# Optimization experiments

Hardware: AMD Instinct MI355X
Metric: run time of the kernel (lower is better)

## Reference

```python
import jax, jax.numpy as jnp
import numpy as np

B, S, E, H, D = 4, 2048, 1024, 16, 64


def setup_inputs() -> dict:
    key = jax.random.key(0)
    ks = jax.random.split(key, 6)
    scale_in = 1.0 / np.sqrt(E)
    return {
        "x": jax.random.normal(ks[0], (B, S, E), dtype=jnp.float32),
        "Wq": jax.random.normal(ks[1], (H, E, D), dtype=jnp.float32) * scale_in,
        "bq": jnp.zeros((H, D), dtype=jnp.float32),
        "Wk": jax.random.normal(ks[2], (H, E, D), dtype=jnp.float32) * scale_in,
        "bk": jnp.zeros((H, D), dtype=jnp.float32),
        "Wv": jax.random.normal(ks[3], (H, E, D), dtype=jnp.float32) * scale_in,
        "bv": jnp.zeros((H, D), dtype=jnp.float32),
        "Wo": jax.random.normal(ks[4], (H * D, E), dtype=jnp.float32) * (1.0 / np.sqrt(H * D)),
        "bo": jnp.zeros((E,), dtype=jnp.float32),
    }


def reference(x, Wq, bq, Wk, bk, Wv, bv, Wo, bo):
    # Per-head Q/K/V projections, batched over heads: [B,S,E] x [H,E,D] -> [B,H,S,D]
    q = jnp.einsum("bse,hed->bhsd", x, Wq) + bq[None, :, None, :]
    k = jnp.einsum("bse,hed->bhsd", x, Wk) + bk[None, :, None, :]
    v = jnp.einsum("bse,hed->bhsd", x, Wv) + bv[None, :, None, :]

    d = q.shape[-1]
    scores = jnp.einsum("bhqd,bhkd->bhqk", q, k) / jnp.sqrt(jnp.asarray(d, q.dtype))
    # Causal mask (registered tril buffer of size max_seq_len in HeadAttention)
    seq = scores.shape[-1]
    causal = jnp.tril(jnp.ones((seq, seq), dtype=bool))
    scores = jnp.where(causal[None, None, :, :], scores, jnp.asarray(-1e9, scores.dtype))
    attn = jax.nn.softmax(scores, axis=-1)
    out = jnp.einsum("bhqk,bhkd->bhqd", attn, v)  # [B,H,S,D]

    # Concat heads: [B,S,H*D], then output projection (dropout is identity in eval)
    out = out.transpose(0, 2, 1, 3).reshape(out.shape[0], out.shape[2], -1)
    return out @ Wo + bo
```

## Files before the change

kernel.cpp:

```cpp
#include <hip/hip_runtime.h>

typedef __bf16 bf16x8 __attribute__((ext_vector_type(8)));
typedef __bf16 bf16x4 __attribute__((ext_vector_type(4)));
typedef float  f32x4  __attribute__((ext_vector_type(4)));

#define B_    4
#define S_    2048
#define E_    1024
#define H_    16
#define D_    64
#define MROWS (B_*S_)
#define HD3   3072

#define SCORE_SCALE 0.18033688011112043f

__device__ __forceinline__ void load_lds16(const void* g, void* l) {
  __builtin_amdgcn_global_load_lds((__attribute__((address_space(1))) void*)g,
                                   (__attribute__((address_space(3))) void*)l,
                                   16, 0, 0);
}

__device__ __forceinline__ f32x4 mfma16(bf16x8 a, bf16x8 b, f32x4 c) {
  return __builtin_amdgcn_mfma_f32_16x16x32_bf16(a, b, c, 0, 0, 0);
}

__device__ __forceinline__ int swz(int row, int dchunk) {
  return row * 64 + ((dchunk ^ (row & 7)) * 8);
}


__global__ void prep(const float4* __restrict__ x, const float* __restrict__ Wq,
                     const float* __restrict__ Wk, const float* __restrict__ Wv,
                     const float* __restrict__ bq, const float* __restrict__ bk,
                     const float* __restrict__ bv, const float* __restrict__ Wo,
                     __bf16* __restrict__ xb, __bf16* __restrict__ Wt,
                     float* __restrict__ bqkv, __bf16* __restrict__ Wot) {
  __shared__ float t[64][65];
  int bid = blockIdx.x;
  if (bid < 8192) {
    int id = bid * 256 + threadIdx.x;
    float4 v = x[id];
    bf16x4 o = { (__bf16)v.x, (__bf16)v.y, (__bf16)v.z, (__bf16)v.w };
    *(bf16x4*)(xb + 4 * (size_t)id) = o;
    return;
  }
  int tx = threadIdx.x & 63;
  int ty = threadIdx.x >> 6;
  if (bid < 8960) {
    int b2 = bid - 8192;
    int e0 = (b2 & 15) * 64;
    int h  = (b2 >> 4) & 15;
    int p  = b2 >> 8;
    const float* W    = (p == 0) ? Wq : (p == 1) ? Wk : Wv;
    const float* bsrc = (p == 0) ? bq : (p == 1) ? bk : bv;
#pragma unroll
    for (int r = 0; r < 16; ++r) {
      int eL = ty + r * 4;
      t[eL][tx] = W[((size_t)h * 1024 + (e0 + eL)) * 64 + tx];
    }
    __syncthreads();
#pragma unroll
    for (int r = 0; r < 16; ++r) {
      int d = ty + r * 4;
      Wt[((size_t)(p * 1024 + h * 64 + d)) * 1024 + e0 + tx] = (__bf16)t[tx][d];
    }
    if ((b2 & 15) == 0 && threadIdx.x < 64)
      bqkv[p * 1024 + h * 64 + threadIdx.x] = bsrc[h * 64 + threadIdx.x];
  } else {
    int b2 = bid - 8960;
    int hd0 = (b2 >> 4) * 64;
    int e0  = (b2 & 15) * 64;
#pragma unroll
    for (int r = 0; r < 16; ++r) {
      int hdL = ty + r * 4;
      t[hdL][tx] = Wo[(size_t)(hd0 + hdL) * 1024 + e0 + tx];
    }
    __syncthreads();
#pragma unroll
    for (int r = 0; r < 16; ++r) {
      int eL = ty + r * 4;
      Wot[(size_t)(e0 + eL) * 1024 + hd0 + tx] = (__bf16)t[tx][eL];
    }
  }
}


template <int MODE>
__global__ __launch_bounds__(256) void gemm_bt(const __bf16* __restrict__ A,
                                               const __bf16* __restrict__ Bt,
                                               const float* __restrict__ bias,
                                               void* __restrict__ Cout,
                                               __bf16* __restrict__ VT,
                                               int M, int N, int K) {
  __shared__ __attribute__((aligned(16))) __bf16 As[128 * 64];
  __shared__ __attribute__((aligned(16))) __bf16 Bs[128 * 64];
  int tid = threadIdx.x, wave = tid >> 6, lane = tid & 63;
  int quad = lane >> 4, cc = lane & 15;
  int nb = N >> 7;
  int nwg = (int)gridDim.x;
  int bid = (int)blockIdx.x;
  bid = (bid & 7) * (nwg >> 3) + (bid >> 3);
  int bm = bid / nb, bn = bid % nb;
  const __bf16* Abase = A + (size_t)bm * 128 * K;
  const __bf16* Bbase = Bt + (size_t)bn * 128 * K;
  int wr = (wave >> 1) * 64, wc = (wave & 1) * 64;
  f32x4 acc[4][4];
#pragma unroll
  for (int i = 0; i < 4; ++i)
#pragma unroll
    for (int j = 0; j < 4; ++j) acc[i][j] = (f32x4){0.f, 0.f, 0.f, 0.f};

  int srow[4], scol[4];
#pragma unroll
  for (int p = 0; p < 4; ++p) {
    int g = tid + p * 256;
    srow[p] = g >> 3;
    scol[p] = ((g & 7) ^ (srow[p] & 7)) * 8;
  }
#pragma unroll
  for (int p = 0; p < 4; ++p) {
    load_lds16(Abase + (size_t)srow[p] * K + scol[p], &As[(tid + p * 256) * 8]);
    load_lds16(Bbase + (size_t)srow[p] * K + scol[p], &Bs[(tid + p * 256) * 8]);
  }

  for (int k0 = 0; k0 < K; k0 += 64) {
    __syncthreads();
    bf16x8 af[2][4], bf[2][4];
#pragma unroll
    for (int kk = 0; kk < 2; ++kk) {
#pragma unroll
      for (int i = 0; i < 4; ++i) af[kk][i] = *(const bf16x8*)&As[swz(wr + i * 16 + cc, kk * 4 + quad)];
#pragma unroll
      for (int j = 0; j < 4; ++j) bf[kk][j] = *(const bf16x8*)&Bs[swz(wc + j * 16 + cc, kk * 4 + quad)];
    }
    __syncthreads();
    if (k0 + 64 < K) {
      int kn = k0 + 64;
#pragma unroll
      for (int p = 0; p < 4; ++p) {
        load_lds16(Abase + (size_t)srow[p] * K + kn + scol[p], &As[(tid + p * 256) * 8]);
        load_lds16(Bbase + (size_t)srow[p] * K + kn + scol[p], &Bs[(tid + p * 256) * 8]);
      }
    }
#pragma unroll
    for (int kk = 0; kk < 2; ++kk)
#pragma unroll
      for (int i = 0; i < 4; ++i)
#pragma unroll
        for (int j = 0; j < 4; ++j) acc[i][j] = mfma16(af[kk][i], bf[kk][j], acc[i][j]);
  }

#pragma unroll
  for (int j = 0; j < 4; ++j) {
    int col = bn * 128 + wc + j * 16 + cc;
    float bv = bias[col];
#pragma unroll
    for (int i = 0; i < 4; ++i) {
      int row0 = bm * 128 + wr + i * 16 + quad * 4;
      if (MODE == 0) {
#pragma unroll
        for (int r = 0; r < 4; ++r)
          ((float*)Cout)[(size_t)(row0 + r) * N + col] = acc[i][j][r] + bv;
      } else if (col < 2048) {
        float sc = (col < 1024) ? SCORE_SCALE : 1.0f;
#pragma unroll
        for (int r = 0; r < 4; ++r)
          ((__bf16*)Cout)[(size_t)(row0 + r) * 2048 + col] = (__bf16)((acc[i][j][r] + bv) * sc);
      } else {
        int bh = (row0 >> 11) * 16 + ((col >> 6) & 15);
        int d  = col & 63;
        bf16x4 pk;
#pragma unroll
        for (int r = 0; r < 4; ++r) pk[r] = (__bf16)(acc[i][j][r] + bv);
        *(bf16x4*)&VT[((size_t)(bh * 64 + d)) * 2048 + (row0 & 2047)] = pk;
      }
    }
  }
}


__global__ __launch_bounds__(256, 3) void attn(const __bf16* __restrict__ QKb,
                                               const __bf16* __restrict__ VT,
                                               __bf16* __restrict__ O) {
  int bx = blockIdx.x;
  int bh = bx & 63;
  int g  = bx >> 6;
  int qt = (g < 8) ? (15 - g) : (g - 8);
  int h  = bh & 15;
  int b  = bh >> 4;
  int q0 = qt * 128;
  int tid = threadIdx.x, wave = tid >> 6, lane = tid & 63;
  int quad = lane >> 4, c = lane & 15;

  __shared__ __attribute__((aligned(16))) __bf16 smem[24576];
  __bf16* Qs = smem;
  __bf16* Ks = smem + 8192;
  __bf16* Vs = smem + 16384;
  __bf16* Ps = smem + wave * 2048;

  const __bf16* Qbase = QKb + (size_t)(b * S_ + q0) * 2048 + h * 64;
  const __bf16* Vbase = VT + (size_t)bh * (64 * 2048);
#pragma unroll
  for (int p = 0; p < 4; ++p) {
    int gi = tid + p * 256;
    int row = gi >> 3, pch = gi & 7;
    load_lds16(Qbase + (size_t)row * 2048 + (pch ^ (row & 7)) * 8, &Qs[gi * 8]);
  }
  {
    const __bf16* Kb = QKb + (size_t)(b * S_) * 2048 + 1024 + h * 64;
#pragma unroll
    for (int p = 0; p < 2; ++p) {
      int gi = tid + p * 256;
      int row = gi >> 3, pch = gi & 7;
      load_lds16(Kb + (size_t)row * 2048 + (pch ^ (row & 7)) * 8, &Ks[gi * 8]);
      load_lds16(Vbase + (size_t)row * 2048 + (pch ^ (row & 7)) * 8, &Vs[gi * 8]);
    }
  }
  __syncthreads();

  bf16x8 qf[2][2];
#pragma unroll
  for (int i = 0; i < 2; ++i)
#pragma unroll
    for (int kk = 0; kk < 2; ++kk)
      qf[i][kk] = *(const bf16x8*)&Qs[swz(wave * 32 + i * 16 + c, kk * 4 + quad)];

  const __bf16 one_b = (__bf16)1.0f;
  bf16x8 ones = { one_b, one_b, one_b, one_b, one_b, one_b, one_b, one_b };

  f32x4 acc_o[2][4], acc_l[2];
#pragma unroll
  for (int i = 0; i < 2; ++i) {
    acc_l[i] = (f32x4){0.f, 0.f, 0.f, 0.f};
#pragma unroll
    for (int j = 0; j < 4; ++j) acc_o[i][j] = (f32x4){0.f, 0.f, 0.f, 0.f};
  }

  int qwave = q0 + wave * 32;
  int ntiles = qt * 2 + 2;
  for (int t = 0; t < ntiles; ++t) {
    int cur = t & 1;
    if (t + 1 < ntiles) {
      int kv1 = (t + 1) * 64;
      const __bf16* Kb = QKb + (size_t)(b * S_ + kv1) * 2048 + 1024 + h * 64;
      const __bf16* Vb = Vbase + kv1;
#pragma unroll
      for (int p = 0; p < 2; ++p) {
        int gi = tid + p * 256;
        int row = gi >> 3, pch = gi & 7;
        load_lds16(Kb + (size_t)row * 2048 + (pch ^ (row & 7)) * 8,
                   &Ks[(cur ^ 1) * 4096 + gi * 8]);
        load_lds16(Vb + (size_t)row * 2048 + (pch ^ (row & 7)) * 8,
                   &Vs[(cur ^ 1) * 4096 + gi * 8]);
      }
    }

    int kv0 = t * 64;
    if (kv0 <= qwave + 31) {
      const __bf16* Kc = Ks + cur * 4096;
      const __bf16* Vc = Vs + cur * 4096;

      f32x4 acc_t[2][4];
#pragma unroll
      for (int i = 0; i < 2; ++i)
#pragma unroll
        for (int j = 0; j < 4; ++j) acc_t[i][j] = (f32x4){0.f, 0.f, 0.f, 0.f};
      bf16x8 kf[4][2];
#pragma unroll
      for (int j = 0; j < 4; ++j)
#pragma unroll
        for (int kk = 0; kk < 2; ++kk)
          kf[j][kk] = *(const bf16x8*)&Kc[swz(j * 16 + c, kk * 4 + quad)];
      __builtin_amdgcn_s_setprio(1);
#pragma unroll
      for (int i = 0; i < 2; ++i)
#pragma unroll
        for (int j = 0; j < 4; ++j)
#pragma unroll
          for (int kk = 0; kk < 2; ++kk)
            acc_t[i][j] = mfma16(kf[j][kk], qf[i][kk], acc_t[i][j]);
      __builtin_amdgcn_s_setprio(0);

      bool domask = (kv0 + 63 > qwave);
#pragma unroll
      for (int i = 0; i < 2; ++i) {
        int q_l = i * 16 + c;
        int q_g = qwave + q_l;
#pragma unroll
        for (int j = 0; j < 4; ++j) {
          bf16x4 pk;
#pragma unroll
          for (int r = 0; r < 4; ++r) {
            float p = __builtin_amdgcn_exp2f(acc_t[i][j][r]);
            if (domask) {
              int kv = kv0 + j * 16 + quad * 4 + r;
              p = (kv > q_g) ? 0.f : p;
            }
            pk[r] = (__bf16)p;
          }
          int dch8 = j * 2 + (quad >> 1);
          int phys = q_l * 64 + ((dch8 ^ (q_l & 7)) * 8) + (quad & 1) * 4;
          *(bf16x4*)&Ps[phys] = pk;
        }
      }

      bf16x8 pf[2][2], vf[4][2];
#pragma unroll
      for (int i = 0; i < 2; ++i)
#pragma unroll
        for (int kk = 0; kk < 2; ++kk)
          pf[i][kk] = *(const bf16x8*)&Ps[swz(i * 16 + c, kk * 4 + quad)];
#pragma unroll
      for (int j = 0; j < 4; ++j)
#pragma unroll
        for (int kk = 0; kk < 2; ++kk)
          vf[j][kk] = *(const bf16x8*)&Vc[swz(j * 16 + c, kk * 4 + quad)];
      __builtin_amdgcn_s_setprio(1);
#pragma unroll
      for (int i = 0; i < 2; ++i) {
#pragma unroll
        for (int j = 0; j < 4; ++j)
#pragma unroll
          for (int kk = 0; kk < 2; ++kk)
            acc_o[i][j] = mfma16(pf[i][kk], vf[j][kk], acc_o[i][j]);
        acc_l[i] = mfma16(pf[i][0], ones, acc_l[i]);
        acc_l[i] = mfma16(pf[i][1], ones, acc_l[i]);
      }
      __builtin_amdgcn_s_setprio(0);
    }

    __syncthreads();
  }

  __bf16* Obase = O + (size_t)(b * S_ + q0) * 1024 + h * 64;
#pragma unroll
  for (int i = 0; i < 2; ++i)
#pragma unroll
    for (int r = 0; r < 4; ++r) {
      float rl = 1.0f / acc_l[i][r];
      int row = wave * 32 + i * 16 + quad * 4 + r;
#pragma unroll
      for (int j = 0; j < 4; ++j)
        Obase[(size_t)row * 1024 + j * 16 + c] = (__bf16)(acc_o[i][j][r] * rl);
    }
}


extern "C" void kernel_launch(void* const* d_in, const int* in_sizes, int n_in,
                              void* d_out, int out_size, void* d_ws, size_t ws_size,
                              hipStream_t stream) {
  (void)in_sizes; (void)n_in; (void)out_size; (void)ws_size;
  const float* x  = (const float*)d_in[0];
  const float* Wq = (const float*)d_in[1];
  const float* bq = (const float*)d_in[2];
  const float* Wk = (const float*)d_in[3];
  const float* bk = (const float*)d_in[4];
  const float* Wv = (const float*)d_in[5];
  const float* bv = (const float*)d_in[6];
  const float* Wo = (const float*)d_in[7];
  const float* bo = (const float*)d_in[8];

  char* w = (char*)d_ws;
  __bf16* xb   = (__bf16*)(w);
  __bf16* Wt   = (__bf16*)(w + (16ull << 20));
  __bf16* Wot  = (__bf16*)(w + (22ull << 20));
  float*  bqkv = (float*) (w + (24ull << 20));
  __bf16* QKb  = (__bf16*)(w + (25ull << 20));
  __bf16* Ob   = (__bf16*)(w + (57ull << 20));
  __bf16* VT   = (__bf16*)(w + (73ull << 20));

  prep   <<<9216, 256, 0, stream>>>((const float4*)x, Wq, Wk, Wv, bq, bk, bv, Wo,
                                    xb, Wt, bqkv, Wot);
  gemm_bt<1><<<dim3((MROWS / 128) * (3072 / 128)), 256, 0, stream>>>(xb, Wt, bqkv, (void*)QKb, VT, MROWS, 3072, 1024);
  attn   <<<1024, 256, 0, stream>>>(QKb, VT, Ob);
  gemm_bt<0><<<dim3((MROWS / 128) * (1024 / 128)), 256, 0, stream>>>(Ob, Wot, bo, d_out, nullptr, MROWS, 1024, 1024);
}
```

Before: 245.5 us.

## Replace GEMM with 8-wave double-buffered ping-pong kernel using larger tiles

Replaces the 4-wave 128x128 GEMM with a 512-thread kernel that computes 256xBN tiles (BN=192 for the QKV projection, 128 for the output projection). It double-buffers A/B in LDS and interleaves the async global->LDS loads with MFMA groups using manual waitcnt, barriers and setprio. The aim is to hide load latency and raise data reuse per tile. In exchange it uses more registers and LDS and relies on fragile hand-scheduled synchronisation, and K=1024 is hardcoded.

```diff
diff --git a/kernel.cpp b/kernel.cpp
--- a/kernel.cpp
+++ b/kernel.cpp
@@ -10,7 +10,6 @@
 #define H_    16
 #define D_    64
 #define MROWS (B_*S_)
-#define HD3   3072
 
 #define SCORE_SCALE 0.18033688011112043f
 
@@ -85,97 +84,153 @@
 }
 
 
-template <int MODE>
-__global__ __launch_bounds__(256) void gemm_bt(const __bf16* __restrict__ A,
-                                               const __bf16* __restrict__ Bt,
-                                               const float* __restrict__ bias,
-                                               void* __restrict__ Cout,
-                                               __bf16* __restrict__ VT,
-                                               int M, int N, int K) {
-  __shared__ __attribute__((aligned(16))) __bf16 As[128 * 64];
-  __shared__ __attribute__((aligned(16))) __bf16 Bs[128 * 64];
+template <int MODE, int BN, int NDIM>
+__global__ __launch_bounds__(512, 2) void gemm8p(const __bf16* __restrict__ A,
+                                                 const __bf16* __restrict__ Bt,
+                                                 const float* __restrict__ bias,
+                                                 void* __restrict__ Cout,
+                                                 __bf16* __restrict__ VT) {
+  constexpr int K = 1024;
+  constexpr int NB = BN / 64;
+  constexpr int WC = BN / 4;
+  __shared__ __attribute__((aligned(16))) __bf16 As[2 * 256 * 64];
+  __shared__ __attribute__((aligned(16))) __bf16 Bs[2 * BN * 64];
+
   int tid = threadIdx.x, wave = tid >> 6, lane = tid & 63;
   int quad = lane >> 4, cc = lane & 15;
-  int nb = N >> 7;
+  constexpr int nb = NDIM / BN;
   int nwg = (int)gridDim.x;
   int bid = (int)blockIdx.x;
   bid = (bid & 7) * (nwg >> 3) + (bid >> 3);
   int bm = bid / nb, bn = bid % nb;
-  const __bf16* Abase = A + (size_t)bm * 128 * K;
-  const __bf16* Bbase = Bt + (size_t)bn * 128 * K;
-  int wr = (wave >> 1) * 64, wc = (wave & 1) * 64;
-  f32x4 acc[4][4];
-#pragma unroll
-  for (int i = 0; i < 4; ++i)
-#pragma unroll
-    for (int j = 0; j < 4; ++j) acc[i][j] = (f32x4){0.f, 0.f, 0.f, 0.f};
-
-  int srow[4], scol[4];
-#pragma unroll
-  for (int p = 0; p < 4; ++p) {
-    int g = tid + p * 256;
-    srow[p] = g >> 3;
-    scol[p] = ((g & 7) ^ (srow[p] & 7)) * 8;
-  }
-#pragma unroll
-  for (int p = 0; p < 4; ++p) {
-    load_lds16(Abase + (size_t)srow[p] * K + scol[p], &As[(tid + p * 256) * 8]);
-    load_lds16(Bbase + (size_t)srow[p] * K + scol[p], &Bs[(tid + p * 256) * 8]);
-  }
-
-  for (int k0 = 0; k0 < K; k0 += 64) {
-    __syncthreads();
-    bf16x8 af[2][4], bf[2][4];
-#pragma unroll
-    for (int kk = 0; kk < 2; ++kk) {
-#pragma unroll
-      for (int i = 0; i < 4; ++i) af[kk][i] = *(const bf16x8*)&As[swz(wr + i * 16 + cc, kk * 4 + quad)];
-#pragma unroll
-      for (int j = 0; j < 4; ++j) bf[kk][j] = *(const bf16x8*)&Bs[swz(wc + j * 16 + cc, kk * 4 + quad)];
-    }
-    __syncthreads();
-    if (k0 + 64 < K) {
-      int kn = k0 + 64;
-#pragma unroll
-      for (int p = 0; p < 4; ++p) {
-        load_lds16(Abase + (size_t)srow[p] * K + kn + scol[p], &As[(tid + p * 256) * 8]);
-        load_lds16(Bbase + (size_t)srow[p] * K + kn + scol[p], &Bs[(tid + p * 256) * 8]);
+  const __bf16* Abase = A + (size_t)bm * 256 * K;
+  const __bf16* Bbase = Bt + (size_t)bn * BN * K;
+  int wrow = (wave >> 2) * 128;
+  int wcol = (wave & 3) * WC;
+
+  f32x4 acc[8][NB];
+#pragma unroll
+  for (int m = 0; m < 8; ++m)
+#pragma unroll
+    for (int n = 0; n < NB; ++n) acc[m][n] = (f32x4){0.f, 0.f, 0.f, 0.f};
+
+  int srl = tid >> 3;
+  int sch = tid & 7;
+  int scol = (sch ^ (srl & 7)) * 8;
+
+#define STAGE_A(t, sub, buf)                                                   \
+  load_lds16(Abase + (size_t)((sub) * 64 + srl) * K + (t) * 64 + scol,         \
+             &As[(buf) * 16384 + (sub) * 4096 + tid * 8])
+#define STAGE_B(t, sub, buf)                                                   \
+  load_lds16(Bbase + (size_t)((sub) * 64 + srl) * K + (t) * 64 + scol,         \
+             &Bs[(buf) * (BN * 64) + (sub) * 4096 + tid * 8])
+
+#pragma unroll
+  for (int s = 0; s < 4; ++s) STAGE_A(0, s, 0);
+#pragma unroll
+  for (int s = 0; s < NB; ++s) STAGE_B(0, s, 0);
+#pragma unroll
+  for (int s = 0; s < 4; ++s) STAGE_A(1, s, 1);
+  asm volatile("s_waitcnt vmcnt(4)" ::: "memory");
+  __builtin_amdgcn_sched_barrier(0);
+  asm volatile("s_barrier" ::: "memory");
+
+  bf16x8 af[8][2], bfr[NB][2];
+
+#define RD_B(buf)                                                              \
+  _Pragma("unroll") for (int n = 0; n < NB; ++n)                               \
+      _Pragma("unroll") for (int kk = 0; kk < 2; ++kk)                         \
+          bfr[n][kk] = *(const bf16x8*)&Bs[(buf) * (BN * 64) +                 \
+                                           swz(wcol + n * 16 + cc, kk * 4 + quad)]
+#define RD_A(buf, mlo)                                                         \
+  _Pragma("unroll") for (int m = mlo; m < (mlo) + 4; ++m)                      \
+      _Pragma("unroll") for (int kk = 0; kk < 2; ++kk)                         \
+          af[m][kk] = *(const bf16x8*)&As[(buf) * 16384 +                      \
+                                          swz(wrow + m * 16 + cc, kk * 4 + quad)]
+#define MFMA_PAIR(q)                                                           \
+  do {                                                                         \
+    __builtin_amdgcn_s_setprio(1);                                             \
+    _Pragma("unroll") for (int m2 = 0; m2 < 2; ++m2)                           \
+        _Pragma("unroll") for (int n = 0; n < NB; ++n)                         \
+            _Pragma("unroll") for (int kk = 0; kk < 2; ++kk)                   \
+                acc[(q) * 2 + m2][n] =                                         \
+                    mfma16(af[(q) * 2 + m2][kk], bfr[n][kk],                   \
+                           acc[(q) * 2 + m2][n]);                              \
+    __builtin_amdgcn_s_setprio(0);                                             \
+  } while (0)
+#define LGKM0                                                                  \
+  asm volatile("s_waitcnt lgkmcnt(0)" ::: "memory");                           \
+  __builtin_amdgcn_sched_barrier(0)
+#define BAR asm volatile("s_barrier" ::: "memory")
+
+#pragma unroll 1
+  for (int it = 0; it < 8; ++it) {
+    int b_t = 2 * it + 1;
+    int c_t = (2 * it + 2) & 15;
+    int d_t = (2 * it + 3) & 15;
+    RD_B(0); RD_A(0, 0);
+    STAGE_B(b_t, 0, 1); STAGE_B(b_t, 1, 1);
+    LGKM0; MFMA_PAIR(0); BAR;
+    RD_A(0, 4);
+    if (NB == 3) STAGE_B(b_t, 2, 1);
+    LGKM0; MFMA_PAIR(1); BAR;
+    STAGE_A(c_t, 0, 0); STAGE_A(c_t, 1, 0);
+    MFMA_PAIR(2); BAR;
+    STAGE_A(c_t, 2, 0); STAGE_A(c_t, 3, 0);
+    MFMA_PAIR(3);
+    asm volatile("s_waitcnt vmcnt(4)" ::: "memory");
+    __builtin_amdgcn_sched_barrier(0);
+    BAR;
+    RD_B(1); RD_A(1, 0);
+    STAGE_B(c_t, 0, 0); STAGE_B(c_t, 1, 0);
+    LGKM0; MFMA_PAIR(0); BAR;
+    RD_A(1, 4);
+    if (NB == 3) STAGE_B(c_t, 2, 0);
+    LGKM0; MFMA_PAIR(1); BAR;
+    STAGE_A(d_t, 0, 1); STAGE_A(d_t, 1, 1);
+    MFMA_PAIR(2); BAR;
+    STAGE_A(d_t, 2, 1); STAGE_A(d_t, 3, 1);
+    MFMA_PAIR(3);
+    asm volatile("s_waitcnt vmcnt(4)" ::: "memory");
+    __builtin_amdgcn_sched_barrier(0);
+    BAR;
+  }
+  asm volatile("s_waitcnt vmcnt(0)" ::: "memory");
+
+#pragma unroll
+  for (int n = 0; n < NB; ++n) {
+    int gcol = bn * BN + wcol + n * 16 + cc;
+    float bv = bias[gcol];
+#pragma unroll
+    for (int m = 0; m < 8; ++m) {
+      int grow0 = bm * 256 + wrow + m * 16 + quad * 4;
+      if (MODE == 0) {
+#pragma unroll
+        for (int r = 0; r < 4; ++r)
+          ((float*)Cout)[(size_t)(grow0 + r) * NDIM + gcol] = acc[m][n][r] + bv;
+      } else if (gcol < 2048) {
+        float sc = (gcol < 1024) ? SCORE_SCALE : 1.0f;
+#pragma unroll
+        for (int r = 0; r < 4; ++r)
+          ((__bf16*)Cout)[(size_t)(grow0 + r) * 2048 + gcol] =
+              (__bf16)((acc[m][n][r] + bv) * sc);
+      } else {
+        int bh = (grow0 >> 11) * 16 + ((gcol >> 6) & 15);
+        int d  = gcol & 63;
+        bf16x4 pk;
+#pragma unroll
+        for (int r = 0; r < 4; ++r) pk[r] = (__bf16)(acc[m][n][r] + bv);
+        *(bf16x4*)&VT[((size_t)(bh * 64 + d)) * 2048 + (grow0 & 2047)] = pk;
       }
     }
-#pragma unroll
-    for (int kk = 0; kk < 2; ++kk)
-#pragma unroll
-      for (int i = 0; i < 4; ++i)
-#pragma unroll
-        for (int j = 0; j < 4; ++j) acc[i][j] = mfma16(af[kk][i], bf[kk][j], acc[i][j]);
-  }
-
-#pragma unroll
-  for (int j = 0; j < 4; ++j) {
-    int col = bn * 128 + wc + j * 16 + cc;
-    float bv = bias[col];
-#pragma unroll
-    for (int i = 0; i < 4; ++i) {
-      int row0 = bm * 128 + wr + i * 16 + quad * 4;
-      if (MODE == 0) {
-#pragma unroll
-        for (int r = 0; r < 4; ++r)
-          ((float*)Cout)[(size_t)(row0 + r) * N + col] = acc[i][j][r] + bv;
-      } else if (col < 2048) {
-        float sc = (col < 1024) ? SCORE_SCALE : 1.0f;
-#pragma unroll
-        for (int r = 0; r < 4; ++r)
-          ((__bf16*)Cout)[(size_t)(row0 + r) * 2048 + col] = (__bf16)((acc[i][j][r] + bv) * sc);
-      } else {
-        int bh = (row0 >> 11) * 16 + ((col >> 6) & 15);
-        int d  = col & 63;
-        bf16x4 pk;
-#pragma unroll
-        for (int r = 0; r < 4; ++r) pk[r] = (__bf16)(acc[i][j][r] + bv);
-        *(bf16x4*)&VT[((size_t)(bh * 64 + d)) * 2048 + (row0 & 2047)] = pk;
-      }
-    }
-  }
+  }
+#undef STAGE_A
+#undef STAGE_B
+#undef RD_B
+#undef RD_A
+#undef MFMA_PAIR
+#undef LGKM0
+#undef BAR
 }
 
 
@@ -369,9 +424,9 @@
   __bf16* Ob   = (__bf16*)(w + (57ull << 20));
   __bf16* VT   = (__bf16*)(w + (73ull << 20));
 
-  prep   <<<9216, 256, 0, stream>>>((const float4*)x, Wq, Wk, Wv, bq, bk, bv, Wo,
-                                    xb, Wt, bqkv, Wot);
-  gemm_bt<1><<<dim3((MROWS / 128) * (3072 / 128)), 256, 0, stream>>>(xb, Wt, bqkv, (void*)QKb, VT, MROWS, 3072, 1024);
-  attn   <<<1024, 256, 0, stream>>>(QKb, VT, Ob);
-  gemm_bt<0><<<dim3((MROWS / 128) * (1024 / 128)), 256, 0, stream>>>(Ob, Wot, bo, d_out, nullptr, MROWS, 1024, 1024);
-}
+  prep<<<9216, 256, 0, stream>>>((const float4*)x, Wq, Wk, Wv, bq, bk, bv, Wo,
+                                 xb, Wt, bqkv, Wot);
+  gemm8p<1, 192, 3072><<<512, 512, 0, stream>>>(xb, Wt, bqkv, (void*)QKb, VT);
+  attn<<<1024, 256, 0, stream>>>(QKb, VT, Ob);
+  gemm8p<0, 128, 1024><<<256, 512, 0, stream>>>(Ob, Wot, bo, d_out, nullptr);
+}
```

Measured after the change: 236.0 us. 3.9% less time.
